# Performance work log

Hardware: AMD Instinct MI355X
Metric: run time of the kernel (lower is better)

Reference implementation:

```python
import jax, jax.numpy as jnp
import numpy as np

N = 150000
E = 1200000
IN_DIM = 64
HID = 64


def setup_inputs() -> dict:
    key = jax.random.key(0)
    k1, k2, k3, k4 = jax.random.split(key, 4)
    obs = jax.random.normal(k1, (N, IN_DIM), dtype=jnp.float32)
    edge_index = jax.random.randint(k2, (2, E), 0, N, dtype=jnp.int64)
    # GCNConv layer params (Glorot-style scale)
    W1 = jax.random.normal(k3, (IN_DIM, HID), dtype=jnp.float32) / jnp.sqrt(IN_DIM)
    b1 = jnp.zeros((HID,), dtype=jnp.float32)
    W2 = jax.random.normal(k4, (HID, 1), dtype=jnp.float32) / jnp.sqrt(HID)
    b2 = jnp.zeros((1,), dtype=jnp.float32)
    return {"obs": obs, "edge_index": edge_index, "W1": W1, "b1": b1, "W2": W2, "b2": b2}


def gcn_conv(x, W, b, src, dst, n):
    # PyG GCNConv: x' = D^{-1/2} (A + I) D^{-1/2} (x W) + b
    x = x @ W  # [N, F_out]
    # degree with self-loops (edge weight 1)
    deg = jax.ops.segment_sum(jnp.ones((src.shape[0],), x.dtype), dst, num_segments=n) + 1.0
    dinv = jax.lax.rsqrt(deg)  # deg >= 1, safe
    norm = dinv[src] * dinv[dst]  # per-edge norm
    msg = x[src] * norm[:, None]  # gather + scale
    agg = jax.ops.segment_sum(msg, dst, num_segments=n)
    agg = agg + x * (dinv * dinv)[:, None]  # self-loop term
    return agg + b


def reference(obs, edge_index, W1, b1, W2, b2):
    src, dst = edge_index[0], edge_index[1]
    h1 = jax.nn.relu(gcn_conv(obs, W1, b1, src, dst, N))
    h2 = jax.nn.relu(gcn_conv(h1, W2, b2, src, dst, N))
    out = h2.reshape(-1, 15)[:, 3:].reshape(-1)
    return out
```

## Files before the change

### kernel.cpp

```cpp
#include <hip/hip_runtime.h>


#define BK 256
#define NBMAX 640
#define EPB 4096
#define HB 320

typedef unsigned int uint;
typedef unsigned short ushort;
typedef __attribute__((ext_vector_type(8))) short bf16x8_t;
typedef __attribute__((ext_vector_type(4))) float f32x4_t;

static __device__ __forceinline__ ushort f2bf(float x) {
    uint u = __float_as_uint(x);
    u = (u + 0x7FFFu + ((u >> 16) & 1u)) >> 16;
    return (ushort)u;
}

__global__ __launch_bounds__(256) void k_hist(const int* __restrict__ dst, int E, int nb,
                                              int* __restrict__ hist) {
    __shared__ int h[NBMAX];
    const int t = threadIdx.x, b = blockIdx.x;
    for (int j = t; j < nb; j += 256) h[j] = 0;
    __syncthreads();
    const int e0 = b * EPB, e1 = min(e0 + EPB, E);
    for (int e = e0 + t; e < e1; e += 256) atomicAdd(&h[dst[e] >> 8], 1);
    __syncthreads();
    for (int j = t; j < nb; j += 256) hist[j * HB + b] = h[j];
}

__global__ __launch_bounds__(256) void k_cscan1(int* __restrict__ hist, int nblk,
                                                int* __restrict__ colsum) {
    __shared__ int s[256];
    const int j = blockIdx.x, t = threadIdx.x;
    int carry = 0;
    for (int base = 0; base < nblk; base += 256) {
        int idx = base + t;
        int v = (idx < nblk) ? hist[j * HB + idx] : 0;
        __syncthreads();
        s[t] = v;
        __syncthreads();
        for (int o = 1; o < 256; o <<= 1) {
            int x = s[t];
            if (t >= o) x += s[t - o];
            __syncthreads();
            s[t] = x;
            __syncthreads();
        }
        if (idx < nblk) hist[j * HB + idx] = carry + s[t] - v;
        carry += s[255];
    }
    if (t == 0) colsum[j] = carry;
}

__global__ __launch_bounds__(1024) void k_cscan2(const int* __restrict__ colsum, int nb, int N,
                                                 int* __restrict__ boff, int* __restrict__ rowptr) {
    __shared__ int s[1024];
    const int t = threadIdx.x;
    int v = (t < nb) ? colsum[t] : 0;
    s[t] = v;
    __syncthreads();
    for (int o = 1; o < 1024; o <<= 1) {
        int x = s[t];
        if (t >= o) x += s[t - o];
        __syncthreads();
        s[t] = x;
        __syncthreads();
    }
    if (t < nb) boff[t] = s[t] - v;
    if (t == nb - 1) { boff[nb] = s[t]; rowptr[N] = s[t]; }
}

__global__ __launch_bounds__(256) void k_place(const int* __restrict__ src, const int* __restrict__ dst,
                                               int E, int nb, const int* __restrict__ hist,
                                               const int* __restrict__ boff, uint* __restrict__ ebuf) {
    __shared__ int cur[NBMAX];
    const int t = threadIdx.x, b = blockIdx.x;
    for (int j = t; j < nb; j += 256) cur[j] = boff[j] + hist[j * HB + b];
    __syncthreads();
    const int e0 = b * EPB, e1 = min(e0 + EPB, E);
    for (int e = e0 + t; e < e1; e += 256) {
        int d = dst[e];
        int p = atomicAdd(&cur[d >> 8], 1);
        ebuf[p] = ((uint)(d & 255) << 24) | (uint)src[e];
    }
}

__global__ __launch_bounds__(256) void k_fill3(const uint* __restrict__ ebuf, const int* __restrict__ boff,
                                               int N, int* __restrict__ rowptr, float* __restrict__ dinv,
                                               int* __restrict__ csrc) {
    __shared__ int cnt[BK];
    __shared__ int sc[BK];
    __shared__ int cur[BK];
    const int b = blockIdx.x, v0 = b << 8, t = threadIdx.x;
    const int nv = min(BK, N - v0);
    cnt[t] = 0;
    __syncthreads();
    const int bb = boff[b], be = boff[b + 1];
    for (int j = bb + t; j < be; j += 256) atomicAdd(&cnt[ebuf[j] >> 24], 1);
    __syncthreads();
    const int c = cnt[t];
    if (t < nv) dinv[v0 + t] = rsqrtf((float)c + 1.0f);
    sc[t] = c;
    __syncthreads();
    for (int o = 1; o < 256; o <<= 1) {
        int x = sc[t];
        if (t >= o) x += sc[t - o];
        __syncthreads();
        sc[t] = x;
        __syncthreads();
    }
    const int ex = sc[t] - c + bb;
    if (t < nv) rowptr[v0 + t] = ex;
    cur[t] = ex;
    __syncthreads();
    for (int j = bb + t; j < be; j += 256) {
        uint e = ebuf[j];
        int p = atomicAdd(&cur[e >> 24], 1);
        csrc[p] = (int)(e & 0xFFFFFFu);
    }
}

__global__ __launch_bounds__(256) void k_gemm1(const float* __restrict__ X, const float* __restrict__ W,
                                               const float* __restrict__ dinv, int N,
                                               ushort* __restrict__ Yh) {
    __shared__ __align__(16) ushort Wt[64 * 72];
    __shared__ __align__(16) ushort Ot[64 * 72];
    const int t = threadIdx.x;

#pragma unroll
    for (int i = 0; i < 4; i++) {
        int idx = t + i * 256;
        int k = idx >> 4;
        int c4 = idx & 15;
        float4 w4 = ((const float4*)W)[idx];
        Wt[(c4 * 4 + 0) * 72 + k] = f2bf(w4.x);
        Wt[(c4 * 4 + 1) * 72 + k] = f2bf(w4.y);
        Wt[(c4 * 4 + 2) * 72 + k] = f2bf(w4.z);
        Wt[(c4 * 4 + 3) * 72 + k] = f2bf(w4.w);
    }
    __syncthreads();

    const int l = t & 63;
    const int lr = l & 15;
    const int g = l >> 4;
    const int wv = t >> 6;

#pragma unroll
    for (int tile = 0; tile < 2; tile++) {
        const int row0 = blockIdx.x * 128 + tile * 64;
        const int rw = row0 + wv * 16;

        bf16x8_t afr[2];
#pragma unroll
        for (int s = 0; s < 2; s++) {
            const int row = rw + lr;
            float4 xa = make_float4(0.f, 0.f, 0.f, 0.f), xb = xa;
            if (row < N) {
                const float4* xp = (const float4*)(X + (size_t)row * 64 + s * 32 + g * 8);
                xa = xp[0];
                xb = xp[1];
            }
            bf16x8_t af;
            af[0] = (short)f2bf(xa.x); af[1] = (short)f2bf(xa.y);
            af[2] = (short)f2bf(xa.z); af[3] = (short)f2bf(xa.w);
            af[4] = (short)f2bf(xb.x); af[5] = (short)f2bf(xb.y);
            af[6] = (short)f2bf(xb.z); af[7] = (short)f2bf(xb.w);
            afr[s] = af;
        }

        const float4 dv = *(const float4*)(dinv + rw + g * 4);

#pragma unroll
        for (int c = 0; c < 4; c++) {
            f32x4_t acc = {0.f, 0.f, 0.f, 0.f};
#pragma unroll
            for (int s = 0; s < 2; s++) {
                const bf16x8_t bf = *(const bf16x8_t*)&Wt[(c * 16 + lr) * 72 + s * 32 + g * 8];
                acc = __builtin_amdgcn_mfma_f32_16x16x32_bf16(afr[s], bf, acc, 0, 0, 0);
            }
            const int col = c * 16 + lr;
#pragma unroll
            for (int r = 0; r < 4; r++) {
                const float sc = (r == 0) ? dv.x : (r == 1) ? dv.y : (r == 2) ? dv.z : dv.w;
                Ot[(wv * 16 + g * 4 + r) * 72 + col] = f2bf(acc[r] * sc);
            }
        }
        __syncthreads();

#pragma unroll
        for (int i = 0; i < 2; i++) {
            int vi = t + i * 256;
            int row = vi >> 3;
            int c8 = vi & 7;
            int grow = row0 + row;
            if (grow < N)
                ((uint4*)(Yh + (size_t)grow * 64))[c8] = *(const uint4*)&Ot[row * 72 + c8 * 8];
        }
        __syncthreads();
    }
}

__global__ __launch_bounds__(256) void k_agg(const ushort* __restrict__ Yh, const int* __restrict__ rowptr,
                                             const int* __restrict__ csrc, const float* __restrict__ dinv,
                                             const float* __restrict__ b1, const float* __restrict__ W2,
                                             int N, float* __restrict__ zs) {
    int t = blockIdx.x * 256 + threadIdx.x;
    int v = t >> 3;
    if (v >= N) return;
    int li = t & 7;
    const uint4* Y4 = (const uint4*)Yh;
    int start = rowptr[v];
    int cnt = rowptr[v + 1] - start;

    float a[8];
    {
        uint4 m = Y4[(size_t)v * 8 + li];
        a[0] = __uint_as_float(m.x << 16);
        a[1] = __uint_as_float(m.x & 0xFFFF0000u);
        a[2] = __uint_as_float(m.y << 16);
        a[3] = __uint_as_float(m.y & 0xFFFF0000u);
        a[4] = __uint_as_float(m.z << 16);
        a[5] = __uint_as_float(m.z & 0xFFFF0000u);
        a[6] = __uint_as_float(m.w << 16);
        a[7] = __uint_as_float(m.w & 0xFFFF0000u);
    }

    int idx = (li < cnt) ? csrc[start + li] : 0;
    for (int j0 = 0; j0 < cnt; j0 += 8) {
        int rem = cnt - j0;
        int nxt = 0;
        if (li < rem - 8) nxt = csrc[start + j0 + 8 + li];
#pragma unroll
        for (int k = 0; k < 8; k++) {
            if (k < rem) {
                int s = __shfl(idx, k, 8);
                uint4 m = Y4[(size_t)s * 8 + li];
                a[0] += __uint_as_float(m.x << 16);
                a[1] += __uint_as_float(m.x & 0xFFFF0000u);
                a[2] += __uint_as_float(m.y << 16);
                a[3] += __uint_as_float(m.y & 0xFFFF0000u);
                a[4] += __uint_as_float(m.z << 16);
                a[5] += __uint_as_float(m.z & 0xFFFF0000u);
                a[6] += __uint_as_float(m.w << 16);
                a[7] += __uint_as_float(m.w & 0xFFFF0000u);
            }
        }
        idx = nxt;
    }

    float dv = dinv[v];
    float4 ba = ((const float4*)b1)[2 * li], bb = ((const float4*)b1)[2 * li + 1];
    float4 wa = ((const float4*)W2)[2 * li], wb = ((const float4*)W2)[2 * li + 1];
    float p;
    p  = fmaxf(fmaf(dv, a[0], ba.x), 0.f) * wa.x;
    p += fmaxf(fmaf(dv, a[1], ba.y), 0.f) * wa.y;
    p += fmaxf(fmaf(dv, a[2], ba.z), 0.f) * wa.z;
    p += fmaxf(fmaf(dv, a[3], ba.w), 0.f) * wa.w;
    p += fmaxf(fmaf(dv, a[4], bb.x), 0.f) * wb.x;
    p += fmaxf(fmaf(dv, a[5], bb.y), 0.f) * wb.y;
    p += fmaxf(fmaf(dv, a[6], bb.z), 0.f) * wb.z;
    p += fmaxf(fmaf(dv, a[7], bb.w), 0.f) * wb.w;
    p += __shfl_xor(p, 1);
    p += __shfl_xor(p, 2);
    p += __shfl_xor(p, 4);
    if (li == 0) zs[v] = p * dv;
}

__global__ __launch_bounds__(256) void k_out2(const float* __restrict__ zs, const int* __restrict__ rowptr,
                                              const int* __restrict__ csrc, const float* __restrict__ dinv,
                                              const float* __restrict__ b2, int M, float* __restrict__ out) {
    int i = blockIdx.x * 256 + threadIdx.x;
    if (i >= M) return;
    int q = i / 12;
    int c = i - q * 12;
    int v = q * 15 + 3 + c;
    int j = rowptr[v];
    const int end = rowptr[v + 1];
    float s = zs[v];
    for (; j + 4 <= end; j += 4) {
        int i0 = csrc[j], i1 = csrc[j + 1], i2 = csrc[j + 2], i3 = csrc[j + 3];
        s += zs[i0] + zs[i1] + zs[i2] + zs[i3];
    }
    for (; j < end; j++) s += zs[csrc[j]];
    out[i] = fmaxf(fmaf(dinv[v], s, b2[0]), 0.f);
}

extern "C" void kernel_launch(void* const* d_in, const int* in_sizes, int n_in,
                              void* d_out, int out_size, void* d_ws, size_t ws_size,
                              hipStream_t stream) {
    const float* obs = (const float*)d_in[0];
    const int*   ei  = (const int*)d_in[1];
    const float* W1  = (const float*)d_in[2];
    const float* b1  = (const float*)d_in[3];
    const float* W2  = (const float*)d_in[4];
    const float* b2  = (const float*)d_in[5];

    const int N = in_sizes[0] / 64;
    const int E = in_sizes[1] / 2;
    const int M = out_size;
    const int NB = (N + BK - 1) / BK;
    const int NBLK = (E + EPB - 1) / EPB;

    const int* src = ei;
    const int* dst = ei + E;

    ushort* Yh     = (ushort*)d_ws;
    float*  dinv   = (float*)(Yh + (size_t)N * 64);
    float*  zs     = dinv + N;
    int*    rowptr = (int*)(zs + N);
    int*    colsum = rowptr + N + 1;
    int*    boff   = colsum + NBMAX;
    int*    hist   = boff + NBMAX + 1;
    uint*   ebuf   = (uint*)(hist + NBMAX * HB);
    int*    csrc   = (int*)(ebuf + E);

    k_hist  <<<NBLK, 256, 0, stream>>>(dst, E, NB, hist);
    k_cscan1<<<NB, 256, 0, stream>>>(hist, NBLK, colsum);
    k_cscan2<<<1, 1024, 0, stream>>>(colsum, NB, N, boff, rowptr);
    k_place <<<NBLK, 256, 0, stream>>>(src, dst, E, NB, hist, boff, ebuf);
    k_fill3 <<<NB, 256, 0, stream>>>(ebuf, boff, N, rowptr, dinv, csrc);
    k_gemm1 <<<(N + 127) / 128, 256, 0, stream>>>(obs, W1, dinv, N, Yh);
    k_agg   <<<((size_t)N * 8 + 255) / 256, 256, 0, stream>>>(Yh, rowptr, csrc, dinv, b1, W2, N, zs);
    k_out2  <<<(M + 255) / 256, 256, 0, stream>>>(zs, rowptr, csrc, dinv, b2, M, (float*)d_out);
}
```

Baseline: 95.59 us.

## Vectorize edge loads, cache bucket edges in LDS, use packed bf16 conversion

```diff
diff --git a/kernel.cpp b/kernel.cpp
--- a/kernel.cpp
+++ b/kernel.cpp
@@ -1,10 +1,12 @@
 #include <hip/hip_runtime.h>
+#include <hip/hip_bf16.h>
 
 
 #define BK 256
 #define NBMAX 640
 #define EPB 4096
 #define HB 320
+#define FCAP 3072
 
 typedef unsigned int uint;
 typedef unsigned short ushort;
@@ -15,6 +17,11 @@
     uint u = __float_as_uint(x);
     u = (u + 0x7FFFu + ((u >> 16) & 1u)) >> 16;
     return (ushort)u;
+}
+
+static __device__ __forceinline__ uint pk2(float a, float b) {
+    __hip_bfloat162 h = __float22bfloat162_rn(make_float2(a, b));
+    return *(uint*)&h;
 }
 
 __global__ __launch_bounds__(256) void k_hist(const int* __restrict__ dst, int E, int nb,
@@ -24,7 +31,18 @@
     for (int j = t; j < nb; j += 256) h[j] = 0;
     __syncthreads();
     const int e0 = b * EPB, e1 = min(e0 + EPB, E);
-    for (int e = e0 + t; e < e1; e += 256) atomicAdd(&h[dst[e] >> 8], 1);
+    if ((((size_t)dst) & 15) == 0) {
+        const int nfull = (e1 - e0) & ~3;
+        const int4* d4 = (const int4*)(dst + e0);
+        for (int i = t; i < (nfull >> 2); i += 256) {
+            int4 d = d4[i];
+            atomicAdd(&h[d.x >> 8], 1); atomicAdd(&h[d.y >> 8], 1);
+            atomicAdd(&h[d.z >> 8], 1); atomicAdd(&h[d.w >> 8], 1);
+        }
+        for (int e = e0 + nfull + t; e < e1; e += 256) atomicAdd(&h[dst[e] >> 8], 1);
+    } else {
+        for (int e = e0 + t; e < e1; e += 256) atomicAdd(&h[dst[e] >> 8], 1);
+    }
     __syncthreads();
     for (int j = t; j < nb; j += 256) hist[j * HB + b] = h[j];
 }
@@ -79,10 +97,30 @@
     for (int j = t; j < nb; j += 256) cur[j] = boff[j] + hist[j * HB + b];
     __syncthreads();
     const int e0 = b * EPB, e1 = min(e0 + EPB, E);
-    for (int e = e0 + t; e < e1; e += 256) {
-        int d = dst[e];
-        int p = atomicAdd(&cur[d >> 8], 1);
-        ebuf[p] = ((uint)(d & 255) << 24) | (uint)src[e];
+    if (((((size_t)dst) | ((size_t)src)) & 15) == 0) {
+        const int nfull = (e1 - e0) & ~3;
+        const int4* d4 = (const int4*)(dst + e0);
+        const int4* s4 = (const int4*)(src + e0);
+        for (int i = t; i < (nfull >> 2); i += 256) {
+            int4 d = d4[i];
+            int4 s = s4[i];
+            int p;
+            p = atomicAdd(&cur[d.x >> 8], 1); ebuf[p] = ((uint)(d.x & 255) << 24) | (uint)s.x;
+            p = atomicAdd(&cur[d.y >> 8], 1); ebuf[p] = ((uint)(d.y & 255) << 24) | (uint)s.y;
+            p = atomicAdd(&cur[d.z >> 8], 1); ebuf[p] = ((uint)(d.z & 255) << 24) | (uint)s.z;
+            p = atomicAdd(&cur[d.w >> 8], 1); ebuf[p] = ((uint)(d.w & 255) << 24) | (uint)s.w;
+        }
+        for (int e = e0 + nfull + t; e < e1; e += 256) {
+            int d = dst[e];
+            int p = atomicAdd(&cur[d >> 8], 1);
+            ebuf[p] = ((uint)(d & 255) << 24) | (uint)src[e];
+        }
+    } else {
+        for (int e = e0 + t; e < e1; e += 256) {
+            int d = dst[e];
+            int p = atomicAdd(&cur[d >> 8], 1);
+            ebuf[p] = ((uint)(d & 255) << 24) | (uint)src[e];
+        }
     }
 }
 
@@ -92,12 +130,18 @@
     __shared__ int cnt[BK];
     __shared__ int sc[BK];
     __shared__ int cur[BK];
+    __shared__ uint se[FCAP];
     const int b = blockIdx.x, v0 = b << 8, t = threadIdx.x;
     const int nv = min(BK, N - v0);
     cnt[t] = 0;
     __syncthreads();
     const int bb = boff[b], be = boff[b + 1];
-    for (int j = bb + t; j < be; j += 256) atomicAdd(&cnt[ebuf[j] >> 24], 1);
+    const int ne = be - bb;
+    for (int j = t; j < ne; j += 256) {
+        uint e = ebuf[bb + j];
+        if (j < FCAP) se[j] = e;
+        atomicAdd(&cnt[e >> 24], 1);
+    }
     __syncthreads();
     const int c = cnt[t];
     if (t < nv) dinv[v0 + t] = rsqrtf((float)c + 1.0f);
@@ -114,8 +158,8 @@
     if (t < nv) rowptr[v0 + t] = ex;
     cur[t] = ex;
     __syncthreads();
-    for (int j = bb + t; j < be; j += 256) {
-        uint e = ebuf[j];
+    for (int j = t; j < ne; j += 256) {
+        uint e = (j < FCAP) ? se[j] : ebuf[bb + j];
         int p = atomicAdd(&cur[e >> 24], 1);
         csrc[p] = (int)(e & 0xFFFFFFu);
     }
@@ -161,12 +205,12 @@
                 xa = xp[0];
                 xb = xp[1];
             }
-            bf16x8_t af;
-            af[0] = (short)f2bf(xa.x); af[1] = (short)f2bf(xa.y);
-            af[2] = (short)f2bf(xa.z); af[3] = (short)f2bf(xa.w);
-            af[4] = (short)f2bf(xb.x); af[5] = (short)f2bf(xb.y);
-            af[6] = (short)f2bf(xb.z); af[7] = (short)f2bf(xb.w);
-            afr[s] = af;
+            uint4 ua;
+            ua.x = pk2(xa.x, xa.y);
+            ua.y = pk2(xa.z, xa.w);
+            ua.z = pk2(xb.x, xb.y);
+            ua.w = pk2(xb.z, xb.w);
+            afr[s] = __builtin_bit_cast(bf16x8_t, ua);
         }
 
         const float4 dv = *(const float4*)(dinv + rw + g * 4);
@@ -180,11 +224,13 @@
                 acc = __builtin_amdgcn_mfma_f32_16x16x32_bf16(afr[s], bf, acc, 0, 0, 0);
             }
             const int col = c * 16 + lr;
-#pragma unroll
-            for (int r = 0; r < 4; r++) {
-                const float sc = (r == 0) ? dv.x : (r == 1) ? dv.y : (r == 2) ? dv.z : dv.w;
-                Ot[(wv * 16 + g * 4 + r) * 72 + col] = f2bf(acc[r] * sc);
-            }
+            const int rb = wv * 16 + g * 4;
+            uint u01 = pk2(acc[0] * dv.x, acc[1] * dv.y);
+            uint u23 = pk2(acc[2] * dv.z, acc[3] * dv.w);
+            Ot[(rb + 0) * 72 + col] = (ushort)(u01 & 0xFFFFu);
+            Ot[(rb + 1) * 72 + col] = (ushort)(u01 >> 16);
+            Ot[(rb + 2) * 72 + col] = (ushort)(u23 & 0xFFFFu);
+            Ot[(rb + 3) * 72 + col] = (ushort)(u23 >> 16);
         }
         __syncthreads();
 
```

After: 89.42 us (median of 2 runs). 1.07x faster.
